# Optimization experiments

Measured on AMD Instinct MI355X. Metric: run time of the kernel, lower is better.

The kernel has to match this reference:

```python
import jax, jax.numpy as jnp
import numpy as np

N_EMBD = 1024
HEAD_SIZE = 64
B, T = 8, 4096


def setup_inputs() -> dict:
    key = jax.random.key(0)
    kx, kk, kq, kv = jax.random.split(key, 4)
    scale = 1.0 / np.sqrt(N_EMBD)
    x = jax.random.normal(kx, (B, T, N_EMBD), dtype=jnp.float32)
    # nn.Linear(N_EMBD, head_size, bias=False) weights, stored as [in, out] for x @ W
    W_k = jax.random.uniform(kk, (N_EMBD, HEAD_SIZE), dtype=jnp.float32, minval=-scale, maxval=scale)
    W_q = jax.random.uniform(kq, (N_EMBD, HEAD_SIZE), dtype=jnp.float32, minval=-scale, maxval=scale)
    W_v = jax.random.uniform(kv, (N_EMBD, HEAD_SIZE), dtype=jnp.float32, minval=-scale, maxval=scale)
    return {"x": x, "W_k": W_k, "W_q": W_q, "W_v": W_v}


def reference(x, W_k, W_q, W_v) -> jnp.ndarray:
    # x: [B,T,E]; projections to [B,T,H]
    k = jnp.einsum("bte,eh->bth", x, W_k)
    q = jnp.einsum("bte,eh->bth", x, W_q)
    v = jnp.einsum("bte,eh->bth", x, W_v)
    H = W_k.shape[1]
    scores = jnp.einsum("bth,bsh->bts", q, k) * (H ** -0.5)  # [B,T,T]
    Tlen = x.shape[1]
    causal = jnp.tril(jnp.ones((Tlen, Tlen), dtype=bool))
    scores = jnp.where(causal, scores, -jnp.inf)
    attn = jax.nn.softmax(scores, axis=-1)
    # dropout is identity in eval mode (deterministic reference)
    return jnp.einsum("bts,bsh->bth", attn, v)
```

## Files before the change

### kernel.cpp

```cpp
#include <hip/hip_runtime.h>
#include <hip/hip_bf16.h>
#include <math.h>


#define BB 8
#define TT 4096
#define EE 1024
#define HH 64
#define NSLOT 160
#define SLOTF 4160

typedef __attribute__((ext_vector_type(8))) short short8;
typedef __attribute__((ext_vector_type(4))) float floatx4;
typedef short8 __attribute__((may_alias)) short8_a;
typedef uint2 __attribute__((may_alias)) uint2_a;
typedef uint4 __attribute__((may_alias)) uint4_a;
typedef float4 __attribute__((may_alias)) float4_a;

#define GLDS(gp, lp)                                                     \
  __builtin_amdgcn_global_load_lds(                                      \
      (const __attribute__((address_space(1))) unsigned int*)(gp),       \
      (__attribute__((address_space(3))) unsigned int*)(lp), 16, 0, 0)

__device__ __forceinline__ unsigned short f2bf(float f) {
  union { float f; unsigned int u; } v; v.f = f;
  unsigned int r = v.u + 0x7fffu + ((v.u >> 16) & 1u);
  return (unsigned short)(r >> 16);
}
__device__ __forceinline__ unsigned int pk2(float a, float b) {
  unsigned int r;
  asm("v_cvt_pk_bf16_f32 %0, %1, %2" : "=v"(r) : "v"(a), "v"(b));
  return r;
}
__device__ __forceinline__ floatx4 fzero() {
  floatx4 z = {0.f, 0.f, 0.f, 0.f};
  return z;
}
__device__ __forceinline__ floatx4 mfma_bf16(short8 a, short8 b, floatx4 c) {
  return __builtin_amdgcn_mfma_f32_16x16x32_bf16(a, b, c, 0, 0, 0);
}
__device__ __forceinline__ short8 pack8(float4 a, float4 b) {
  union { unsigned int u[4]; short8 s; } r;
  r.u[0] = pk2(a.x, a.y);
  r.u[1] = pk2(a.z, a.w);
  r.u[2] = pk2(b.x, b.y);
  r.u[3] = pk2(b.z, b.w);
  return r.s;
}

__global__ __launch_bounds__(256) void wt_kernel(
    const float* __restrict__ Wk, const float* __restrict__ Wq,
    const float* __restrict__ Wv, unsigned short* __restrict__ wt3) {
  __shared__ float tile[64][65];
  const int m = blockIdx.y;
  const int eb = blockIdx.x;
  const float* W = (m == 0) ? Wk : ((m == 1) ? Wq : Wv);
  const int t = threadIdx.x;
  {
    const int r = t >> 2;
    const int c0 = (t & 3) * 16;
    const float* src = W + (size_t)(eb * 64 + r) * 64 + c0;
#pragma unroll
    for (int i = 0; i < 16; ++i) tile[r][c0 + i] = src[i];
  }
  __syncthreads();
  {
    const int h = t >> 2;
    const int e0 = (t & 3) * 16;
    unsigned int w[8];
#pragma unroll
    for (int i = 0; i < 8; ++i)
      w[i] = pk2(tile[e0 + 2 * i][h], tile[e0 + 2 * i + 1][h]);
    unsigned short* dst = wt3 + (size_t)(m * 64 + h) * EE + eb * 64 + e0;
    ((uint4_a*)dst)[0] = make_uint4(w[0], w[1], w[2], w[3]);
    ((uint4_a*)(dst + 8))[0] = make_uint4(w[4], w[5], w[6], w[7]);
  }
}

__global__ __launch_bounds__(256) void proj_kernel(
    const float* __restrict__ x, const unsigned short* __restrict__ wt3,
    unsigned short* __restrict__ kws, unsigned short* __restrict__ qws,
    unsigned short* __restrict__ vtws) {
  __shared__ __align__(16) unsigned char LB[3][12288];
  const int t = threadIdx.x;
  const int wv = t >> 6, lane = t & 63;
  const int l16 = lane & 15, quad = lane >> 4;
  const int mshalf = wv & 1;
  const int jbase = (wv >> 1) * 6;
  const size_t row0 = (size_t)blockIdx.x * 64;

  floatx4 acc[6][2];
#pragma unroll
  for (int j = 0; j < 6; ++j)
#pragma unroll
    for (int m2 = 0; m2 < 2; ++m2) acc[j][m2] = fzero();

  const float* xbase = x + (row0 + mshalf * 32 + l16) * EE + quad * 8;

#define STAGE_B(bufp, cc)                                                      \
  {                                                                            \
    _Pragma("unroll") for (int i = 0; i < 3; ++i) {                            \
      const int idx = wv * 3 + i;                                              \
      const unsigned short* gp =                                               \
          wt3 + (size_t)(idx * 16 + l16) * EE + (cc) * 32 + quad * 8;          \
      GLDS(gp, (bufp) + idx * 1024);                                           \
    }                                                                          \
  }

  float4 ra[2][2], rb[2][2];
#pragma unroll
  for (int m2 = 0; m2 < 2; ++m2)
#pragma unroll
    for (int h = 0; h < 2; ++h)
      ra[m2][h] = *(const float4_a*)(xbase + (size_t)m2 * 16 * EE + h * 4);

  STAGE_B(&LB[0][0], 0);
  STAGE_B(&LB[1][0], 1);
  asm volatile("s_waitcnt vmcnt(3)" ::: "memory");
  __builtin_amdgcn_s_barrier();
  __builtin_amdgcn_sched_barrier(0);

  int cur = 0;
  for (int c = 0; c < 32; ++c) {
    if (c + 1 < 32) {
#pragma unroll
      for (int m2 = 0; m2 < 2; ++m2)
#pragma unroll
        for (int h = 0; h < 2; ++h)
          rb[m2][h] = *(const float4_a*)(xbase + (size_t)m2 * 16 * EE +
                                         (c + 1) * 32 + h * 4);
    }
    if (c + 2 < 32) {
      int sb = cur + 2;
      if (sb >= 3) sb -= 3;
      STAGE_B(&LB[sb][0], c + 2);
    }
    short8 af[2];
#pragma unroll
    for (int m2 = 0; m2 < 2; ++m2) af[m2] = pack8(ra[m2][0], ra[m2][1]);
    const unsigned char* Bb = &LB[cur][0];
#pragma unroll
    for (int jj = 0; jj < 6; ++jj) {
      short8 bfv = *(const short8_a*)(Bb + (size_t)(jbase + jj) * 1024 +
                                      lane * 16);
#pragma unroll
      for (int m2 = 0; m2 < 2; ++m2)
        acc[jj][m2] = mfma_bf16(af[m2], bfv, acc[jj][m2]);
    }
    if (c < 31) {
      if (c + 2 < 32) {
        asm volatile("s_waitcnt vmcnt(3)" ::: "memory");
      } else {
        asm volatile("s_waitcnt vmcnt(0)" ::: "memory");
      }
      __builtin_amdgcn_s_barrier();
      __builtin_amdgcn_sched_barrier(0);
#pragma unroll
      for (int m2 = 0; m2 < 2; ++m2)
#pragma unroll
        for (int h = 0; h < 2; ++h) ra[m2][h] = rb[m2][h];
    }
    cur = (cur == 2) ? 0 : cur + 1;
  }
#undef STAGE_B

  const int b = (int)(row0 >> 12);
  const int tt0 = (int)(row0 & (TT - 1));
#pragma unroll
  for (int j = 0; j < 6; ++j) {
    const int jg = jbase + j;
    const int m = jg >> 2;
    const int h0 = (jg & 3) * 16;
#pragma unroll
    for (int m2 = 0; m2 < 2; ++m2) {
      floatx4 a = acc[j][m2];
      const int rbase = mshalf * 32 + m2 * 16 + quad * 4;
      if (m == 0) {
#pragma unroll
        for (int r = 0; r < 4; ++r)
          kws[(row0 + rbase + r) * HH + h0 + l16] = f2bf(a[r]);
      } else if (m == 1) {
#pragma unroll
        for (int r = 0; r < 4; ++r)
          qws[(row0 + rbase + r) * HH + h0 + l16] = f2bf(a[r] * 0.18033688011112042f);
      } else {
        uint2 p;
        p.x = pk2(a[0], a[1]);
        p.y = pk2(a[2], a[3]);
        ((uint2_a*)&vtws[(size_t)(b * 64 + h0 + l16) * TT + tt0 + rbase])[0] = p;
      }
    }
  }
}

template <bool SPLIT>
__global__ __launch_bounds__(256) void attn_kernel(
    const unsigned short* __restrict__ kws, const unsigned short* __restrict__ qws,
    const unsigned short* __restrict__ vtws, float* __restrict__ dst) {
  __shared__ unsigned short KV[2][16][512];
  __shared__ unsigned short pb[4][16][72];
  const int t = threadIdx.x;
  const int wv = t >> 6, lane = t & 63;
  const int l16 = lane & 15, quad = lane >> 4;
  const int id = (int)blockIdx.x;
  int b, jq, kt0, kt1;
  if (SPLIT) {
    b = id & 7;
    const int cid = id >> 3;
    int s, S;
    if (cid < 16) {
      jq = cid; s = 0; S = 1;
    } else if (cid < 48) {
      const int u = cid - 16; jq = 16 + (u >> 1); s = u & 1; S = 2;
    } else if (cid < 96) {
      const int u = cid - 48; const int d = u / 3; jq = 32 + d; s = u - 3 * d; S = 3;
    } else {
      const int u = cid - 96; jq = 48 + (u >> 2); s = u & 3; S = 4;
    }
    const int n = jq + 1;
    kt0 = (s * n) / S;
    kt1 = ((s + 1) * n) / S;
  } else {
    const int r255 = id & 255;
    b = r255 & 7;
    const int m = r255 >> 3;
    jq = (id < 256) ? m : 63 - m;
    kt0 = 0;
    kt1 = jq + 1;
  }
  const int q0 = jq * 64;
  const int qrow = q0 + wv * 16 + l16;

  const unsigned short* qp = qws + ((size_t)b * TT + qrow) * HH + quad * 8;
  short8 qa0 = *(const short8_a*)(qp);
  short8 qa1 = *(const short8_a*)(qp + 32);

  floatx4 o[4];
#pragma unroll
  for (int nt = 0; nt < 4; ++nt) o[nt] = fzero();
  float lsum = 0.f;

#define STAGE_KV(buf, ks)                                                      \
  {                                                                            \
    _Pragma("unroll") for (int i = 0; i < 4; ++i) {                            \
      const int idx = wv * 4 + i;                                              \
      const unsigned short* gp;                                                \
      if (idx < 8) {                                                           \
        const int nt = idx >> 1, f = idx & 1;                                  \
        gp = kws + ((size_t)b * TT + (ks) + nt * 16 + l16) * HH + f * 32 +     \
             quad * 8;                                                         \
      } else {                                                                 \
        const int nt = (idx - 8) >> 1, f = idx & 1;                            \
        gp = vtws + ((size_t)(b * 64 + nt * 16 + l16)) * TT + (ks) + f * 32 +  \
             quad * 8;                                                         \
      }                                                                        \
      GLDS(gp, &KV[buf][idx][0]);                                              \
    }                                                                          \
  }

  STAGE_KV(0, kt0 * 64);
  __syncthreads();

  for (int kt = kt0; kt < kt1; ++kt) {
    const int cur = (kt - kt0) & 1;
    const int ks = kt * 64;
    if (kt + 1 < kt1) STAGE_KV(cur ^ 1, ks + 64);

    floatx4 sc[4];
#pragma unroll
    for (int nt = 0; nt < 4; ++nt) {
      short8 kf0 = *(const short8_a*)&KV[cur][nt * 2][lane * 8];
      short8 kf1 = *(const short8_a*)&KV[cur][nt * 2 + 1][lane * 8];
      floatx4 z = fzero();
      z = mfma_bf16(kf0, qa0, z);
      z = mfma_bf16(kf1, qa1, z);
      sc[nt] = z;
    }
    if (kt == jq) {
#pragma unroll
      for (int nt = 0; nt < 4; ++nt)
#pragma unroll
        for (int r = 0; r < 4; ++r) {
          const int key = ks + nt * 16 + quad * 4 + r;
          if (key > qrow) sc[nt][r] = -1e30f;
        }
    }
#pragma unroll
    for (int nt = 0; nt < 4; ++nt) {
      const float p0 = exp2f(sc[nt][0]);
      const float p1 = exp2f(sc[nt][1]);
      const float p2 = exp2f(sc[nt][2]);
      const float p3 = exp2f(sc[nt][3]);
      lsum += (p0 + p1) + (p2 + p3);
      uint2 pw;
      pw.x = pk2(p0, p1);
      pw.y = pk2(p2, p3);
      ((uint2_a*)&pb[wv][l16][nt * 16 + quad * 4])[0] = pw;
    }
    short8 pf0 = *(const short8_a*)&pb[wv][l16][quad * 8];
    short8 pf1 = *(const short8_a*)&pb[wv][l16][quad * 8 + 32];
#pragma unroll
    for (int nt = 0; nt < 4; ++nt) {
      short8 vf0 = *(const short8_a*)&KV[cur][8 + nt * 2][lane * 8];
      short8 vf1 = *(const short8_a*)&KV[cur][8 + nt * 2 + 1][lane * 8];
      o[nt] = mfma_bf16(vf0, pf0, o[nt]);
      o[nt] = mfma_bf16(vf1, pf1, o[nt]);
    }
    __syncthreads();
  }
#undef STAGE_KV

  float lr = lsum;
  lr += __shfl_xor(lr, 16);
  lr += __shfl_xor(lr, 32);

  if (SPLIT) {
    float* op = dst + (size_t)id * SLOTF;
    const int ql = wv * 16 + l16;
#pragma unroll
    for (int nt = 0; nt < 4; ++nt) {
      float4 st;
      st.x = o[nt][0];
      st.y = o[nt][1];
      st.z = o[nt][2];
      st.w = o[nt][3];
      *(float4_a*)&op[(size_t)ql * 64 + nt * 16 + quad * 4] = st;
    }
    if (lane < 16) op[4096 + wv * 16 + lane] = lr;
  } else {
    const float inv = 1.0f / lr;
#pragma unroll
    for (int nt = 0; nt < 4; ++nt) {
      float4 st;
      st.x = o[nt][0] * inv;
      st.y = o[nt][1] * inv;
      st.z = o[nt][2] * inv;
      st.w = o[nt][3] * inv;
      *(float4_a*)&dst[((size_t)b * TT + qrow) * HH + nt * 16 + quad * 4] = st;
    }
  }
}

__global__ __launch_bounds__(256) void comb_kernel(
    const float* __restrict__ part, float* __restrict__ out) {
  const int id = (int)blockIdx.x;
  const int b = id & 7;
  const int jq = id >> 3;
  const int tq = jq >> 4;
  const int S = tq + 1;
  const int P = 8 * tq * (tq + 1) + (jq & 15) * S;
  const int t = threadIdx.x;
  const int r0 = t >> 6;
  const int h = t & 63;
  const float* s0 = part + (size_t)(b + 8 * P) * SLOTF;
  const size_t sstr = (size_t)8 * SLOTF;

#pragma unroll 4
  for (int i = 0; i < 16; ++i) {
    const int r = i * 4 + r0;
    float acc = 0.f, l = 0.f;
    for (int s2 = 0; s2 < S; ++s2) {
      acc += s0[(size_t)s2 * sstr + (size_t)r * 64 + h];
      l += s0[(size_t)s2 * sstr + 4096 + r];
    }
    out[((size_t)b * TT + jq * 64 + r) * HH + h] = acc / l;
  }
}

extern "C" void kernel_launch(void* const* d_in, const int* in_sizes, int n_in,
                              void* d_out, int out_size, void* d_ws, size_t ws_size,
                              hipStream_t stream) {
  const float* x = (const float*)d_in[0];
  const float* Wk = (const float*)d_in[1];
  const float* Wq = (const float*)d_in[2];
  const float* Wv = (const float*)d_in[3];
  float* out = (float*)d_out;

  unsigned short* kws = (unsigned short*)d_ws;
  unsigned short* qws = kws + (size_t)BB * TT * HH;
  unsigned short* vtws = qws + (size_t)BB * TT * HH;
  unsigned short* wt3 = vtws + (size_t)BB * TT * HH;
  float* part = (float*)(wt3 + (size_t)3 * HH * EE);

  const size_t base_bytes = (size_t)3 * BB * TT * HH * 2 + (size_t)3 * HH * EE * 2;
  const size_t need = base_bytes + (size_t)BB * NSLOT * SLOTF * 4;
  const bool use_split = (ws_size >= need);

  hipLaunchKernelGGL(wt_kernel, dim3(16, 3), dim3(256), 0, stream, Wk, Wq, Wv, wt3);
  hipLaunchKernelGGL(proj_kernel, dim3(512), dim3(256), 0, stream, x, wt3, kws, qws,
                     vtws);
  if (use_split) {
    hipLaunchKernelGGL((attn_kernel<true>), dim3(BB * NSLOT), dim3(256), 0, stream,
                       kws, qws, vtws, part);
    hipLaunchKernelGGL(comb_kernel, dim3(512), dim3(256), 0, stream, part, out);
  } else {
    hipLaunchKernelGGL((attn_kernel<false>), dim3(512), dim3(256), 0, stream,
                       kws, qws, vtws, out);
  }
}
```

Measured before the change: 293.5 us.

## Prefetch x tiles in groups of four k-chunks with ping-pong register buffers

The QKV projection loop now loads the fp32 x activations four k-chunks at a time into a pair of register buffers, one ahead of use, instead of prefetching a single chunk per iteration. This deepens the global-load pipeline and aims to hide the latency of reading x. The vmcnt waits are adjusted so the grouped loads can stay in flight across the weight LDS stages. The cost is much higher register pressure (two groups of 16 float4s), which may reduce occupancy, and the hand-counted vmcnt values must match the actual load counts.

Measured after the change: 290.4 us. About the same (-1.1%).

```diff
diff --git a/kernel.cpp b/kernel.cpp
--- a/kernel.cpp
+++ b/kernel.cpp
@@ -107,13 +107,18 @@
     }                                                                          \
   }
 
-  float4 ra[2][2], rb[2][2];
-#pragma unroll
-  for (int m2 = 0; m2 < 2; ++m2)
-#pragma unroll
-    for (int h = 0; h < 2; ++h)
-      ra[m2][h] = *(const float4_a*)(xbase + (size_t)m2 * 16 * EE + h * 4);
-
+  float4 GA[4][2][2], GB[4][2][2];
+
+#define LOAD_GROUP(DST, g)                                                     \
+  {                                                                            \
+    _Pragma("unroll") for (int s = 0; s < 4; ++s)                              \
+    _Pragma("unroll") for (int m2 = 0; m2 < 2; ++m2)                           \
+    _Pragma("unroll") for (int h = 0; h < 2; ++h)                              \
+      DST[s][m2][h] = *(const float4_a*)(xbase + (size_t)m2 * 16 * EE +        \
+                                         (g) * 128 + s * 32 + h * 4);          \
+  }
+
+  LOAD_GROUP(GA, 0);
   STAGE_B(&LB[0][0], 0);
   STAGE_B(&LB[1][0], 1);
   asm volatile("s_waitcnt vmcnt(3)" ::: "memory");
@@ -121,47 +126,50 @@
   __builtin_amdgcn_sched_barrier(0);
 
   int cur = 0;
-  for (int c = 0; c < 32; ++c) {
-    if (c + 1 < 32) {
-#pragma unroll
-      for (int m2 = 0; m2 < 2; ++m2)
-#pragma unroll
-        for (int h = 0; h < 2; ++h)
-          rb[m2][h] = *(const float4_a*)(xbase + (size_t)m2 * 16 * EE +
-                                         (c + 1) * 32 + h * 4);
-    }
-    if (c + 2 < 32) {
-      int sb = cur + 2;
-      if (sb >= 3) sb -= 3;
-      STAGE_B(&LB[sb][0], c + 2);
-    }
-    short8 af[2];
-#pragma unroll
-    for (int m2 = 0; m2 < 2; ++m2) af[m2] = pack8(ra[m2][0], ra[m2][1]);
-    const unsigned char* Bb = &LB[cur][0];
-#pragma unroll
-    for (int jj = 0; jj < 6; ++jj) {
-      short8 bfv = *(const short8_a*)(Bb + (size_t)(jbase + jj) * 1024 +
-                                      lane * 16);
-#pragma unroll
-      for (int m2 = 0; m2 < 2; ++m2)
-        acc[jj][m2] = mfma_bf16(af[m2], bfv, acc[jj][m2]);
-    }
-    if (c < 31) {
-      if (c + 2 < 32) {
-        asm volatile("s_waitcnt vmcnt(3)" ::: "memory");
-      } else {
-        asm volatile("s_waitcnt vmcnt(0)" ::: "memory");
-      }
-      __builtin_amdgcn_s_barrier();
-      __builtin_amdgcn_sched_barrier(0);
-#pragma unroll
-      for (int m2 = 0; m2 < 2; ++m2)
-#pragma unroll
-        for (int h = 0; h < 2; ++h) ra[m2][h] = rb[m2][h];
-    }
-    cur = (cur == 2) ? 0 : cur + 1;
-  }
+
+#define GROUP_BODY(CUR, NXT, g)                                                \
+  {                                                                            \
+    if ((g) < 7) LOAD_GROUP(NXT, (g) + 1);                                     \
+    _Pragma("unroll") for (int s = 0; s < 4; ++s) {                            \
+      const int c = 4 * (g) + s;                                               \
+      if (c + 2 < 32) {                                                        \
+        int sb = cur + 2;                                                      \
+        if (sb >= 3) sb -= 3;                                                  \
+        STAGE_B(&LB[sb][0], c + 2);                                            \
+      }                                                                        \
+      short8 af[2];                                                            \
+      _Pragma("unroll") for (int m2 = 0; m2 < 2; ++m2)                         \
+        af[m2] = pack8(CUR[s][m2][0], CUR[s][m2][1]);                          \
+      const unsigned char* Bb = &LB[cur][0];                                   \
+      _Pragma("unroll") for (int jj = 0; jj < 6; ++jj) {                       \
+        short8 bfv = *(const short8_a*)(Bb + (size_t)(jbase + jj) * 1024 +     \
+                                        lane * 16);                            \
+        _Pragma("unroll") for (int m2 = 0; m2 < 2; ++m2)                       \
+          acc[jj][m2] = mfma_bf16(af[m2], bfv, acc[jj][m2]);                   \
+      }                                                                        \
+      if (c < 31) {                                                            \
+        if (s == 0 && (g) < 7) {                                               \
+                     \
+          asm volatile("s_waitcnt vmcnt(19)" ::: "memory");                    \
+        } else if (c + 2 < 32) {                                               \
+                              \
+          asm volatile("s_waitcnt vmcnt(3)" ::: "memory");                     \
+        } else {                                                               \
+          asm volatile("s_waitcnt vmcnt(0)" ::: "memory");                     \
+        }                                                                      \
+        __builtin_amdgcn_s_barrier();                                         \
+        __builtin_amdgcn_sched_barrier(0);                                     \
+      }                                                                        \
+      cur = (cur == 2) ? 0 : cur + 1;                                          \
+    }                                                                          \
+  }
+
+  for (int gp = 0; gp < 4; ++gp) {
+    GROUP_BODY(GA, GB, 2 * gp);
+    GROUP_BODY(GB, GA, 2 * gp + 1);
+  }
+#undef GROUP_BODY
+#undef LOAD_GROUP
 #undef STAGE_B
 
   const int b = (int)(row0 >> 12);
```
